# Performance work log

Hardware: AMD Instinct MI355X
Metric: run time of the kernel (lower is better)

Reference implementation:

```python
import jax, jax.numpy as jnp
import numpy as np

N_LAYERS = 24  # number of recurrent applications of the shared HashLinear


def setup_inputs() -> dict:
    key = jax.random.key(0)
    ks = jax.random.split(key, 9)
    B, D_IN, N, N_OUT = 1024, 784, 4096, 10
    s_in = 1.0 / np.sqrt(D_IN)
    s_h = 1.0 / np.sqrt(N)
    x = jax.random.normal(ks[0], (B, D_IN), jnp.float32)
    # nn.Linear(prod(input_dim), 2*n_units)
    W_in = jax.random.uniform(ks[1], (2 * N, D_IN), jnp.float32, -s_in, s_in)
    b_in = jax.random.uniform(ks[2], (2 * N,), jnp.float32, -s_in, s_in)
    # HashLinear(n_units, n_units, period=1, 'hash'): learnable +/-1 context key + shared linear
    key_sp = jnp.where(jax.random.bernoulli(ks[3], 0.5, (1, N)), 1.0, -1.0).astype(jnp.float32)
    W_sp = jax.random.uniform(ks[4], (N, N), jnp.float32, -s_h, s_h)
    b_sp = jax.random.uniform(ks[5], (N,), jnp.float32, -s_h, s_h)
    # HashLinear(n_units, 10, period=1, 'hash')
    key_f = jnp.where(jax.random.bernoulli(ks[6], 0.5, (1, N)), 1.0, -1.0).astype(jnp.float32)
    W_f = jax.random.uniform(ks[7], (N_OUT, N), jnp.float32, -s_h, s_h)
    b_f = jax.random.uniform(ks[8], (N_OUT,), jnp.float32, -s_h, s_h)
    return {"x": x, "W_in": W_in, "b_in": b_in, "key_sp": key_sp, "W_sp": W_sp,
            "b_sp": b_sp, "key_f": key_f, "W_f": W_f, "b_f": b_f, "time": 0}


def _hash_linear(xa, xb, o, W, b):
    # Superposition HashLinear: same shared weight applied to both streams,
    # each modulated by the +/-1 context key o ([n_in]).
    ya = (xa * o) @ W.T + b
    yb = (xb * o) @ W.T + b
    return ya, yb


def reference(x, W_in, b_in, key_sp, W_sp, b_sp, key_f, W_f, b_f, time):
    N = W_sp.shape[0]
    r = x @ W_in.T + b_in                 # [B, 2N]
    r_a, r_b = r[:, :N], r[:, N:]         # torch.split(r, n_units, 1)
    pre0 = r_a
    r_a, r_b = jax.nn.relu(r_a), jax.nn.relu(r_b)
    o = key_sp[time % key_sp.shape[0]]    # period=1, time=0 in the module

    def step(carry, _):
        a, b2 = carry
        ya, yb = _hash_linear(a, b2, o, W_sp, b_sp)
        return (jax.nn.relu(ya), jax.nn.relu(yb)), ya  # collect preactivation r_a

    (r_a, r_b), pres = jax.lax.scan(step, (r_a, r_b), None, length=N_LAYERS)
    of = key_f[time % key_f.shape[0]]
    out_a, out_b = _hash_linear(r_a, r_b, of, W_f, b_f)  # [B,10], [B,10]
    preactivations = jnp.concatenate([pre0[None], pres], axis=0)  # [N_LAYERS+1, B, N]
    return (out_a, out_b, preactivations)
```

## Files before the change

kernel.cpp:

```cpp
#include <hip/hip_runtime.h>
#include <hip/hip_bf16.h>
#include <stdint.h>

typedef __bf16 bf16x8 __attribute__((ext_vector_type(8)));
typedef float  f32x4  __attribute__((ext_vector_type(4)));
typedef unsigned short ushort8v __attribute__((ext_vector_type(8)));

#define NH      4096
#define MB      1024
#define M2      2048
#define DIN     784
#define KPAD    832
#define N_IN    8192
#define NLAYERS 24
#define NOUT    10

#define ASLE    8192
#define BOFF    (3 * ASLE)

__device__ __forceinline__ unsigned short f2bf(float x) {
  union { float f; unsigned u; } v; v.f = x;
  unsigned r = v.u + 0x7FFFu + ((v.u >> 16) & 1u);
  return (unsigned short)(r >> 16);
}
__device__ __forceinline__ float bf2f(unsigned short u) {
  union { unsigned u; float f; } v; v.u = ((unsigned)u) << 16; return v.f;
}

__device__ __forceinline__ void async16(const void* g, void* l) {
  __builtin_amdgcn_global_load_lds(
      (const __attribute__((address_space(1))) void*)g,
      (__attribute__((address_space(3))) void*)l, 16, 0, 0);
}

__global__ void k_conv_wsp(const float* __restrict__ W, const float* __restrict__ o,
                           unsigned short* __restrict__ out) {
  size_t i = ((size_t)blockIdx.x * blockDim.x + threadIdx.x) * 4;
  if (i >= (size_t)NH * NH) return;
  float4 w = *reinterpret_cast<const float4*>(W + i);
  int k = (int)(i & (NH - 1));
  float4 ov = *reinterpret_cast<const float4*>(o + k);
  ushort4 r;
  r.x = f2bf(w.x * ov.x); r.y = f2bf(w.y * ov.y);
  r.z = f2bf(w.z * ov.z); r.w = f2bf(w.w * ov.w);
  *reinterpret_cast<ushort4*>(out + i) = r;
}

__global__ void k_conv_pad2(const float* __restrict__ Win, const float* __restrict__ x,
                            unsigned short* __restrict__ Win_bf,
                            unsigned short* __restrict__ X_bf) {
  size_t i = (size_t)blockIdx.x * blockDim.x + threadIdx.x;
  if (i >= (size_t)(N_IN + MB) * KPAD) return;
  int r = (int)(i / KPAD), c = (int)(i % KPAD);
  if (r < N_IN) Win_bf[i] = (c < DIN) ? f2bf(Win[(size_t)r * DIN + c]) : (unsigned short)0;
  else {
    int rr = r - N_IN;
    X_bf[(size_t)rr * KPAD + c] = (c < DIN) ? f2bf(x[(size_t)rr * DIN + c]) : (unsigned short)0;
  }
}

__device__ __forceinline__ void gemm_core(
    const unsigned short* __restrict__ Ag, const unsigned short* __restrict__ Bg,
    int K, int bm, int bn, unsigned short* lds, f32x4 acc[4][4])
{
  const int t    = threadIdx.x;
  const int lane = t & 63;
  const int wave = t >> 6;
  const int wm   = wave >> 1;
  const int wn   = wave & 1;
  const int l15  = lane & 15;
  const int lkb  = (lane >> 4) * 16;

  const int srow = t >> 3;
  const int sb   = ((t & 7) * 16) ^ ((srow & 7) << 4);
  const unsigned aG0 = (unsigned)((bm + srow) * K + (sb >> 1));
  const unsigned bG0 = (unsigned)((bn + srow) * K + (sb >> 1));

  auto STAGE_A = [&](int sA, int k0) {
    unsigned short* s = lds + sA * ASLE;
#pragma unroll
    for (int j = 0; j < 4; ++j)
      async16(Ag + aG0 + (unsigned)(j * 32 * K + k0), s + t * 8 + j * 2048);
  };
  auto STAGE_B = [&](int sB, int k0) {
    unsigned short* s = lds + BOFF + sB * ASLE;
#pragma unroll
    for (int j = 0; j < 4; ++j)
      async16(Bg + bG0 + (unsigned)(j * 32 * K + k0), s + t * 8 + j * 2048);
  };

  int aRd[2][4], bRd[2][4];
#pragma unroll
  for (int kk = 0; kk < 2; ++kk)
#pragma unroll
    for (int i = 0; i < 4; ++i) {
      const int ra = wm * 64 + i * 16 + l15;
      aRd[kk][i] = (ra * 128 + ((kk * 64 + lkb) ^ ((ra & 7) << 4))) >> 1;
      const int rb = wn * 64 + i * 16 + l15;
      bRd[kk][i] = (rb * 128 + ((kk * 64 + lkb) ^ ((rb & 7) << 4))) >> 1;
    }

  const int nt = K >> 6;
  STAGE_A(0, 0);
  STAGE_B(0, 0);
  if (nt > 1) STAGE_A(1, 64);

  int sA = 0, sA2 = 2, sB = 0;
  for (int kt = 0; kt < nt; ++kt) {
    if (kt + 1 < nt) asm volatile("s_waitcnt vmcnt(4)" ::: "memory");
    else             asm volatile("s_waitcnt vmcnt(0)" ::: "memory");
    __builtin_amdgcn_s_barrier();
    if (kt + 1 < nt) STAGE_B(sB ^ 1, (kt + 1) << 6);
    if (kt + 2 < nt) STAGE_A(sA2, (kt + 2) << 6);
    const unsigned short* baseA = lds + sA * ASLE;
    const unsigned short* baseB = lds + BOFF + sB * ASLE;
    bf16x8 a[2][4], b[2][4];
#pragma unroll
    for (int kk = 0; kk < 2; ++kk) {
#pragma unroll
      for (int i = 0; i < 4; ++i) a[kk][i] = *reinterpret_cast<const bf16x8*>(baseA + aRd[kk][i]);
#pragma unroll
      for (int i = 0; i < 4; ++i) b[kk][i] = *reinterpret_cast<const bf16x8*>(baseB + bRd[kk][i]);
    }
    __builtin_amdgcn_s_setprio(1);
#pragma unroll
    for (int kk = 0; kk < 2; ++kk)
#pragma unroll
      for (int mi = 0; mi < 4; ++mi)
#pragma unroll
        for (int ni = 0; ni < 4; ++ni)
          acc[mi][ni] = __builtin_amdgcn_mfma_f32_16x16x32_bf16(a[kk][mi], b[kk][ni], acc[mi][ni], 0, 0, 0);
    __builtin_amdgcn_s_setprio(0);
    sA  = (sA  == 2) ? 0 : sA  + 1;
    sA2 = (sA2 == 2) ? 0 : sA2 + 1;
    sB ^= 1;
  }
}

__global__ __launch_bounds__(256, 2) void k_gemm_layer(
    const unsigned short* __restrict__ A, const unsigned short* __restrict__ W,
    const float* __restrict__ bias, float* __restrict__ preact,
    unsigned short* __restrict__ Anext)
{
  __shared__ __align__(16) unsigned short lds[5 * ASLE];
  const int bid = blockIdx.x;
  const int xcd = bid & 7;
  const int idx = bid >> 3;
  const int bm  = (idx >> 2) * 128;
  const int bn  = (xcd * 4 + (idx & 3)) * 128;
  f32x4 acc[4][4] = {};
  gemm_core(A, W, NH, bm, bn, lds, acc);

  const int lane = threadIdx.x & 63;
  const int wave = threadIdx.x >> 6;
  const int wm = (wave >> 1) * 64, wn = (wave & 1) * 64;
  const int l15 = lane & 15;
#pragma unroll
  for (int mi = 0; mi < 4; ++mi) {
    const int gm0 = bm + wm + mi * 16 + (lane >> 4) * 4;
#pragma unroll
    for (int ni = 0; ni < 4; ++ni) {
      const int gn = bn + wn + ni * 16 + l15;
      const float bv = bias[gn];
#pragma unroll
      for (int r = 0; r < 4; ++r) {
        const int gm = gm0 + r;
        const float y = acc[mi][ni][r] + bv;
        if (gm < MB) preact[(size_t)gm * NH + gn] = y;
        Anext[(size_t)gm * NH + gn] = f2bf(y > 0.f ? y : 0.f);
      }
    }
  }
}

__global__ __launch_bounds__(256, 2) void k_gemm_in(
    const unsigned short* __restrict__ X, const unsigned short* __restrict__ W,
    const float* __restrict__ bias, float* __restrict__ preact0,
    unsigned short* __restrict__ A0)
{
  __shared__ __align__(16) unsigned short lds[5 * ASLE];
  const int bid = blockIdx.x;
  const int xcd = bid & 7;
  const int idx = bid >> 3;
  const int bm  = (idx >> 3) * 128;
  const int bn  = (xcd * 8 + (idx & 7)) * 128;
  f32x4 acc[4][4] = {};
  gemm_core(X, W, KPAD, bm, bn, lds, acc);

  const int lane = threadIdx.x & 63;
  const int wave = threadIdx.x >> 6;
  const int wm = (wave >> 1) * 64, wn = (wave & 1) * 64;
  const int l15 = lane & 15;
#pragma unroll
  for (int mi = 0; mi < 4; ++mi) {
    const int gm0 = bm + wm + mi * 16 + (lane >> 4) * 4;
#pragma unroll
    for (int ni = 0; ni < 4; ++ni) {
      const int gn = bn + wn + ni * 16 + l15;
      const float bv = bias[gn];
#pragma unroll
      for (int r = 0; r < 4; ++r) {
        const int gm = gm0 + r;
        const float y = acc[mi][ni][r] + bv;
        const unsigned short rl = f2bf(y > 0.f ? y : 0.f);
        if (gn < NH) {
          preact0[(size_t)gm * NH + gn] = y;
          A0[(size_t)gm * NH + gn] = rl;
        } else {
          A0[(size_t)(MB + gm) * NH + (gn - NH)] = rl;
        }
      }
    }
  }
}

__global__ __launch_bounds__(256) void k_final(
    const unsigned short* __restrict__ A, const float* __restrict__ Wf,
    const float* __restrict__ of, const float* __restrict__ bf_,
    float* __restrict__ out)
{
  __shared__ float red[4][NOUT];
  const int t = threadIdx.x;
  for (int rr = 0; rr < 8; ++rr) {
    const int m = blockIdx.x * 8 + rr;
    float accj[NOUT];
#pragma unroll
    for (int j = 0; j < NOUT; ++j) accj[j] = 0.f;
    for (int k0 = t * 8; k0 < NH; k0 += 256 * 8) {
      const ushort8v av = *reinterpret_cast<const ushort8v*>(A + (size_t)m * NH + k0);
      const float4 o0 = *reinterpret_cast<const float4*>(of + k0);
      const float4 o1 = *reinterpret_cast<const float4*>(of + k0 + 4);
      float a[8];
      a[0] = bf2f(av[0]) * o0.x; a[1] = bf2f(av[1]) * o0.y;
      a[2] = bf2f(av[2]) * o0.z; a[3] = bf2f(av[3]) * o0.w;
      a[4] = bf2f(av[4]) * o1.x; a[5] = bf2f(av[5]) * o1.y;
      a[6] = bf2f(av[6]) * o1.z; a[7] = bf2f(av[7]) * o1.w;
#pragma unroll
      for (int j = 0; j < NOUT; ++j) {
        const float4 w0 = *reinterpret_cast<const float4*>(Wf + (size_t)j * NH + k0);
        const float4 w1 = *reinterpret_cast<const float4*>(Wf + (size_t)j * NH + k0 + 4);
        accj[j] += a[0]*w0.x + a[1]*w0.y + a[2]*w0.z + a[3]*w0.w
                 + a[4]*w1.x + a[5]*w1.y + a[6]*w1.z + a[7]*w1.w;
      }
    }
#pragma unroll
    for (int j = 0; j < NOUT; ++j) {
      float v = accj[j];
      for (int off = 32; off > 0; off >>= 1) v += __shfl_down(v, off);
      if ((t & 63) == 0) red[t >> 6][j] = v;
    }
    __syncthreads();
    if (t < NOUT)
      out[(size_t)m * NOUT + t] = red[0][t] + red[1][t] + red[2][t] + red[3][t] + bf_[t];
    __syncthreads();
  }
}

extern "C" void kernel_launch(void* const* d_in, const int* in_sizes, int n_in,
                              void* d_out, int out_size, void* d_ws, size_t ws_size,
                              hipStream_t stream) {
  const float* x     = (const float*)d_in[0];
  const float* W_in  = (const float*)d_in[1];
  const float* b_in  = (const float*)d_in[2];
  const float* keysp = (const float*)d_in[3];
  const float* W_sp  = (const float*)d_in[4];
  const float* b_sp  = (const float*)d_in[5];
  const float* keyf  = (const float*)d_in[6];
  const float* W_f   = (const float*)d_in[7];
  const float* b_f   = (const float*)d_in[8];

  float* out    = (float*)d_out;
  float* preact = out + (size_t)2 * MB * NOUT;

  char* ws = (char*)d_ws;
  unsigned short* Wsp_bf = (unsigned short*)ws;  ws += (size_t)NH * NH * 2;
  unsigned short* A0     = (unsigned short*)ws;  ws += (size_t)M2 * NH * 2;
  unsigned short* A1     = (unsigned short*)ws;  ws += (size_t)M2 * NH * 2;
  unsigned short* Win_bf = (unsigned short*)ws;  ws += (size_t)N_IN * KPAD * 2;
  unsigned short* X_bf   = (unsigned short*)ws;  ws += (size_t)MB * KPAD * 2;

  k_conv_wsp<<<(NH * (size_t)NH / 4 + 255) / 256, 256, 0, stream>>>(W_sp, keysp, Wsp_bf);
  k_conv_pad2<<<((size_t)(N_IN + MB) * KPAD + 255) / 256, 256, 0, stream>>>(
      W_in, x, Win_bf, X_bf);

  k_gemm_in<<<512, 256, 0, stream>>>(X_bf, Win_bf, b_in, preact, A0);

  unsigned short* Ain = A0;
  unsigned short* Aout = A1;
  for (int tlay = 0; tlay < NLAYERS; ++tlay) {
    float* pre = preact + (size_t)(tlay + 1) * MB * NH;
    k_gemm_layer<<<512, 256, 0, stream>>>(Ain, Wsp_bf, b_sp, pre, Aout);
    unsigned short* tmp = Ain; Ain = Aout; Aout = tmp;
  }

  k_final<<<M2 / 8, 256, 0, stream>>>(Ain, W_f, keyf, b_f, out);
}
```

Measured before the change: 1.517 ms.

## Load B operand directly from global into registers, bypassing LDS

The weight (B) tiles are now read from global memory straight into registers, with a one-step register double buffer (bC/bN), instead of being staged asynchronously through LDS. This removes the B LDS buffers, cutting shared memory from five slices to three, and drops the LDS reads for B. In exchange each wave loads its own B fragments with 16-byte strided global loads, which are less coalesced and duplicated across waves that share columns. It also raises register pressure and puts global latency directly in front of the MFMA loop. The waitcnt and barrier placement moves to match the new pipeline.

```diff
diff --git a/kernel.cpp b/kernel.cpp
--- a/kernel.cpp
+++ b/kernel.cpp
@@ -16,7 +16,6 @@
 #define NOUT    10
 
 #define ASLE    8192
-#define BOFF    (3 * ASLE)
 
 __device__ __forceinline__ unsigned short f2bf(float x) {
   union { float f; unsigned u; } v; v.f = x;
@@ -70,11 +69,11 @@
   const int wn   = wave & 1;
   const int l15  = lane & 15;
   const int lkb  = (lane >> 4) * 16;
+  const int lke  = (lane >> 4) * 8;
 
   const int srow = t >> 3;
   const int sb   = ((t & 7) * 16) ^ ((srow & 7) << 4);
   const unsigned aG0 = (unsigned)((bm + srow) * K + (sb >> 1));
-  const unsigned bG0 = (unsigned)((bn + srow) * K + (sb >> 1));
 
   auto STAGE_A = [&](int sA, int k0) {
     unsigned short* s = lds + sA * ASLE;
@@ -82,46 +81,58 @@
     for (int j = 0; j < 4; ++j)
       async16(Ag + aG0 + (unsigned)(j * 32 * K + k0), s + t * 8 + j * 2048);
   };
-  auto STAGE_B = [&](int sB, int k0) {
-    unsigned short* s = lds + BOFF + sB * ASLE;
-#pragma unroll
-    for (int j = 0; j < 4; ++j)
-      async16(Bg + bG0 + (unsigned)(j * 32 * K + k0), s + t * 8 + j * 2048);
-  };
-
-  int aRd[2][4], bRd[2][4];
+
+  int aRd[2][4];
 #pragma unroll
   for (int kk = 0; kk < 2; ++kk)
 #pragma unroll
     for (int i = 0; i < 4; ++i) {
       const int ra = wm * 64 + i * 16 + l15;
       aRd[kk][i] = (ra * 128 + ((kk * 64 + lkb) ^ ((ra & 7) << 4))) >> 1;
-      const int rb = wn * 64 + i * 16 + l15;
-      bRd[kk][i] = (rb * 128 + ((kk * 64 + lkb) ^ ((rb & 7) << 4))) >> 1;
-    }
+    }
+
+  unsigned bOffE[2][4];
+#pragma unroll
+  for (int kk = 0; kk < 2; ++kk)
+#pragma unroll
+    for (int i = 0; i < 4; ++i)
+      bOffE[kk][i] = (unsigned)((bn + wn * 64 + i * 16 + l15) * K + kk * 32 + lke);
+
+  bf16x8 bC[2][4], bN[2][4];
 
   const int nt = K >> 6;
+#pragma unroll
+  for (int kk = 0; kk < 2; ++kk)
+#pragma unroll
+    for (int i = 0; i < 4; ++i)
+      bC[kk][i] = *reinterpret_cast<const bf16x8*>(Bg + bOffE[kk][i]);
   STAGE_A(0, 0);
-  STAGE_B(0, 0);
-  if (nt > 1) STAGE_A(1, 64);
-
-  int sA = 0, sA2 = 2, sB = 0;
+  if (nt > 1) {
+    STAGE_A(1, 64);
+    asm volatile("s_waitcnt vmcnt(4)" ::: "memory");
+  } else {
+    asm volatile("s_waitcnt vmcnt(0)" ::: "memory");
+  }
+  __builtin_amdgcn_s_barrier();
+
+  int sA = 0, sA2 = 2;
   for (int kt = 0; kt < nt; ++kt) {
-    if (kt + 1 < nt) asm volatile("s_waitcnt vmcnt(4)" ::: "memory");
-    else             asm volatile("s_waitcnt vmcnt(0)" ::: "memory");
-    __builtin_amdgcn_s_barrier();
-    if (kt + 1 < nt) STAGE_B(sB ^ 1, (kt + 1) << 6);
+    if (kt + 1 < nt) {
+      const unsigned ka = (unsigned)((kt + 1) << 6);
+#pragma unroll
+      for (int kk = 0; kk < 2; ++kk)
+#pragma unroll
+        for (int i = 0; i < 4; ++i)
+          bN[kk][i] = *reinterpret_cast<const bf16x8*>(Bg + bOffE[kk][i] + ka);
+    }
     if (kt + 2 < nt) STAGE_A(sA2, (kt + 2) << 6);
     const unsigned short* baseA = lds + sA * ASLE;
-    const unsigned short* baseB = lds + BOFF + sB * ASLE;
-    bf16x8 a[2][4], b[2][4];
-#pragma unroll
-    for (int kk = 0; kk < 2; ++kk) {
-#pragma unroll
-      for (int i = 0; i < 4; ++i) a[kk][i] = *reinterpret_cast<const bf16x8*>(baseA + aRd[kk][i]);
-#pragma unroll
-      for (int i = 0; i < 4; ++i) b[kk][i] = *reinterpret_cast<const bf16x8*>(baseB + bRd[kk][i]);
-    }
+    bf16x8 a[2][4];
+#pragma unroll
+    for (int kk = 0; kk < 2; ++kk)
+#pragma unroll
+      for (int i = 0; i < 4; ++i)
+        a[kk][i] = *reinterpret_cast<const bf16x8*>(baseA + aRd[kk][i]);
     __builtin_amdgcn_s_setprio(1);
 #pragma unroll
     for (int kk = 0; kk < 2; ++kk)
@@ -129,11 +140,20 @@
       for (int mi = 0; mi < 4; ++mi)
 #pragma unroll
         for (int ni = 0; ni < 4; ++ni)
-          acc[mi][ni] = __builtin_amdgcn_mfma_f32_16x16x32_bf16(a[kk][mi], b[kk][ni], acc[mi][ni], 0, 0, 0);
+          acc[mi][ni] = __builtin_amdgcn_mfma_f32_16x16x32_bf16(a[kk][mi], bC[kk][ni], acc[mi][ni], 0, 0, 0);
     __builtin_amdgcn_s_setprio(0);
+    if (kt + 1 < nt) {
+#pragma unroll
+      for (int kk = 0; kk < 2; ++kk)
+#pragma unroll
+        for (int i = 0; i < 4; ++i)
+          bC[kk][i] = bN[kk][i];
+      if (kt + 2 < nt) asm volatile("s_waitcnt vmcnt(4)" ::: "memory");
+      else             asm volatile("s_waitcnt vmcnt(0)" ::: "memory");
+      __builtin_amdgcn_s_barrier();
+    }
     sA  = (sA  == 2) ? 0 : sA  + 1;
     sA2 = (sA2 == 2) ? 0 : sA2 + 1;
-    sB ^= 1;
   }
 }
 
@@ -142,7 +162,7 @@
     const float* __restrict__ bias, float* __restrict__ preact,
     unsigned short* __restrict__ Anext)
 {
-  __shared__ __align__(16) unsigned short lds[5 * ASLE];
+  __shared__ __align__(16) unsigned short lds[3 * ASLE];
   const int bid = blockIdx.x;
   const int xcd = bid & 7;
   const int idx = bid >> 3;
@@ -178,7 +198,7 @@
     const float* __restrict__ bias, float* __restrict__ preact0,
     unsigned short* __restrict__ A0)
 {
-  __shared__ __align__(16) unsigned short lds[5 * ASLE];
+  __shared__ __align__(16) unsigned short lds[3 * ASLE];
   const int bid = blockIdx.x;
   const int xcd = bid & 7;
   const int idx = bid >> 3;
```

Result: slower. 3.421 ms (+125.4%).
